# Performance work log

Measured on AMD Instinct MI355X. Metric: run time of the kernel, lower is better.

Reference implementation:

```python
import jax, jax.numpy as jnp
import numpy as np

N_ATOMS = 8192
N_EDGES = 262144
N_MOL = 128
F = 128
R = 20
CUTOFF = 5.0
L = 3
EPS = 1e-8


def setup_inputs() -> dict:
    key = jax.random.key(0)
    ks = jax.random.split(key, 20)
    sc = 0.05  # weight init scale for numerical stability
    inp = {
        "z": jax.random.randint(ks[0], (N_ATOMS,), 0, 100, dtype=jnp.int32),
        "pos": jax.random.uniform(ks[1], (N_ATOMS, 3), dtype=jnp.float32),
        "edge_src": jax.random.randint(ks[2], (N_EDGES,), 0, N_ATOMS, dtype=jnp.int32),
        "edge_dst": jax.random.randint(ks[3], (N_EDGES,), 0, N_ATOMS, dtype=jnp.int32),
        "mol_idx": jnp.sort(jax.random.randint(ks[4], (N_ATOMS,), 0, N_MOL, dtype=jnp.int32)),
        "embed": jax.random.normal(ks[5], (100, F), dtype=jnp.float32) * sc,
        "msg_w1": jax.random.normal(ks[6], (L, F, F), dtype=jnp.float32) * sc,
        "msg_b1": jnp.zeros((L, F), jnp.float32),
        "msg_w2": jax.random.normal(ks[7], (L, F, 3 * F), dtype=jnp.float32) * sc,
        "msg_b2": jnp.zeros((L, 3 * F), jnp.float32),
        "rbf_w": jax.random.normal(ks[8], (L, R, 3 * F), dtype=jnp.float32) * sc,
        "rbf_b": jnp.zeros((L, 3 * F), jnp.float32),
        "upd_u": jax.random.normal(ks[9], (L, F, F), dtype=jnp.float32) * sc,
        "upd_v": jax.random.normal(ks[10], (L, F, F), dtype=jnp.float32) * sc,
        "upd_a1": jax.random.normal(ks[11], (L, 2 * F, F), dtype=jnp.float32) * sc,
        "upd_a1b": jnp.zeros((L, F), jnp.float32),
        "upd_a2": jax.random.normal(ks[12], (L, F, 3 * F), dtype=jnp.float32) * sc,
        "upd_a2b": jnp.zeros((L, 3 * F), jnp.float32),
        "out_w1": jax.random.normal(ks[13], (F, F), dtype=jnp.float32) * sc,
        "out_b1": jnp.zeros((F,), jnp.float32),
        "out_w2": jax.random.normal(ks[14], (F, 1), dtype=jnp.float32) * sc,
        "out_b2": jnp.zeros((1,), jnp.float32),
    }
    return inp


def _painn_forward(z, pos, edge_src, edge_dst, mol_idx, embed,
                   msg_w1, msg_b1, msg_w2, msg_b2, rbf_w, rbf_b,
                   upd_u, upd_v, upd_a1, upd_a1b, upd_a2, upd_a2b,
                   out_w1, out_b1, out_w2, out_b2):
    n = z.shape[0]
    s = embed[z]                                  # [N,F]
    v = jnp.zeros((n, 3, F), s.dtype)             # [N,3,F]

    rij = pos[edge_dst] - pos[edge_src]           # [E,3]
    d = jnp.sqrt(jnp.sum(rij * rij, axis=-1) + EPS)  # [E]
    unit = rij / d[:, None]                       # [E,3]
    freq = jnp.arange(1, R + 1, dtype=s.dtype) * (jnp.pi / CUTOFF)
    rbf = jnp.sin(d[:, None] * freq[None, :]) / d[:, None]          # [E,R]
    fc = 0.5 * (jnp.cos(jnp.pi * d / CUTOFF) + 1.0) * (d < CUTOFF)  # [E]

    for l in range(L):
        # --- message block ---
        phi = jax.nn.silu(s @ msg_w1[l] + msg_b1[l]) @ msg_w2[l] + msg_b2[l]  # [N,3F]
        wfilt = (rbf @ rbf_w[l] + rbf_b[l]) * fc[:, None]                      # [E,3F]
        m = phi[edge_src] * wfilt                                              # [E,3F]
        ds_e, dvv, dvs = m[:, :F], m[:, F:2 * F], m[:, 2 * F:]
        ds = jax.ops.segment_sum(ds_e, edge_dst, num_segments=n)
        dv_e = v[edge_src] * dvv[:, None, :] + unit[:, :, None] * dvs[:, None, :]  # [E,3,F]
        dv = jax.ops.segment_sum(dv_e, edge_dst, num_segments=n)
        s = s + ds
        v = v + dv
        # --- update block ---
        uv = jnp.einsum('ncf,fg->ncg', v, upd_u[l])   # [N,3,F]
        vv = jnp.einsum('ncf,fg->ncg', v, upd_v[l])   # [N,3,F]
        vv_norm = jnp.sqrt(jnp.sum(vv * vv, axis=1) + EPS)  # [N,F]
        a = jax.nn.silu(jnp.concatenate([s, vv_norm], axis=-1) @ upd_a1[l] + upd_a1b[l])
        a = a @ upd_a2[l] + upd_a2b[l]                # [N,3F]
        a_vv, a_sv, a_ss = a[:, :F], a[:, F:2 * F], a[:, 2 * F:]
        s = s + a_ss + a_sv * jnp.sum(uv * vv, axis=1)
        v = v + a_vv[:, None, :] * uv

    atom_out = jax.nn.silu(s @ out_w1 + out_b1) @ out_w2 + out_b2  # [N,1]
    return jax.ops.segment_sum(atom_out, mol_idx, num_segments=N_MOL)  # [M,1]


def reference(z, pos, edge_src, edge_dst, mol_idx, embed,
              msg_w1, msg_b1, msg_w2, msg_b2, rbf_w, rbf_b,
              upd_u, upd_v, upd_a1, upd_a1b, upd_a2, upd_a2b,
              out_w1, out_b1, out_w2, out_b2):
    return _painn_forward(z, pos, edge_src, edge_dst, mol_idx, embed,
                          msg_w1, msg_b1, msg_w2, msg_b2, rbf_w, rbf_b,
                          upd_u, upd_v, upd_a1, upd_a1b, upd_a2, upd_a2b,
                          out_w1, out_b1, out_w2, out_b2)
```

## Files before the change

### kernel.cpp

```cpp
#include <hip/hip_runtime.h>
#include <hip/hip_bf16.h>
#include <math.h>

#define N_ATOMS 8192
#define N_EDGES 262144
#define N_MOL   128
#define FDIM    128
#define RDIM    20
#define LLAYERS 3
#define CUTOFF  5.0f
#define EPSV    1e-8f
#define PI_F    3.14159265358979323846f

typedef __attribute__((ext_vector_type(8))) short bf16x8;
typedef __attribute__((ext_vector_type(4))) float f32x4;

__device__ __forceinline__ ushort f2bf(float x) {
    uint b = __float_as_uint(x);
    return (ushort)((b + 0x7fffu + ((b >> 16) & 1u)) >> 16);
}

__global__ void k_wconv(const float* __restrict__ w1, const float* __restrict__ w2,
                        const float* __restrict__ uu, const float* __restrict__ uvw,
                        const float* __restrict__ a1, const float* __restrict__ a2,
                        const float* __restrict__ ow1, ushort* __restrict__ WT) {
    int i = blockIdx.x * 256 + threadIdx.x;
    float v;
    if (i < 49152) {
        int idx = i; int l = idx >> 14; idx &= 16383;
        int n = idx >> 7, k = idx & 127;
        v = w1[l*16384 + k*128 + n];
    } else if (i < 196608) {
        int idx = i - 49152; int l = idx / 49152; idx -= l * 49152;
        int n = idx >> 7, k = idx & 127;
        v = w2[l*49152 + k*384 + n];
    } else if (i < 294912) {
        int idx = i - 196608; int l = idx >> 15; idx &= 32767;
        int n = idx >> 7, k = idx & 127;
        v = (n < 128) ? uu[l*16384 + k*128 + n] : uvw[l*16384 + k*128 + (n-128)];
    } else if (i < 393216) {
        int idx = i - 294912; int l = idx >> 15; idx &= 32767;
        int n = idx >> 8, k = idx & 255;
        v = a1[l*32768 + k*128 + n];
    } else if (i < 540672) {
        int idx = i - 393216; int l = idx / 49152; idx -= l * 49152;
        int n = idx >> 7, k = idx & 127;
        v = a2[l*49152 + k*384 + n];
    } else {
        int idx = i - 540672;
        int n = idx >> 7, k = idx & 127;
        v = ow1[k*128 + n];
    }
    WT[i] = f2bf(v);
}

__global__ void k_embed(const int* __restrict__ z, const float* __restrict__ embed,
                        float* __restrict__ S, ushort* __restrict__ SBF) {
    int i = blockIdx.x * 256 + threadIdx.x;
    int a = i >> 7, k = i & 127;
    float v = embed[(size_t)z[a] * FDIM + k];
    S[i] = v; SBF[i] = f2bf(v);
}

__global__ void k_hist(const int* __restrict__ edst, int* __restrict__ CNT) {
    int e = blockIdx.x * 256 + threadIdx.x;
    if (e < N_EDGES) atomicAdd(&CNT[edst[e]], 1);
}

__global__ __launch_bounds__(1024) void k_scan(const int* __restrict__ CNT,
                                               int* __restrict__ OFF, int* __restrict__ CUR) {
    __shared__ int part[1024];
    int t = threadIdx.x;
    int loc[8];
    int run = 0;
    #pragma unroll
    for (int i = 0; i < 8; i++) { int c = CNT[t*8 + i]; loc[i] = run; run += c; }
    part[t] = run;
    __syncthreads();
    for (int off = 1; off < 1024; off <<= 1) {
        int v = 0;
        if (t >= off) v = part[t - off];
        __syncthreads();
        part[t] += v;
        __syncthreads();
    }
    int ebase = (t > 0) ? part[t-1] : 0;
    #pragma unroll
    for (int i = 0; i < 8; i++) { int o = ebase + loc[i]; OFF[t*8+i] = o; CUR[t*8+i] = o; }
    if (t == 1023) OFF[8192] = part[1023];
}

__global__ void k_pos(const int* __restrict__ edst, int* __restrict__ CUR,
                      int* __restrict__ POS) {
    int e = blockIdx.x * 256 + threadIdx.x;
    if (e < N_EDGES) POS[e] = atomicAdd(&CUR[edst[e]], 1);
}

__global__ void k_edges(const float* __restrict__ pos, const int* __restrict__ esrc,
                        const int* __restrict__ edst, const int* __restrict__ POS,
                        float* __restrict__ RBF, float* __restrict__ UNITFC,
                        int* __restrict__ SRCS) {
    int e = blockIdx.x * 256 + threadIdx.x;
    if (e >= N_EDGES) return;
    int s = esrc[e], d = edst[e];
    int p = POS[e];
    float rx = pos[d*3+0] - pos[s*3+0];
    float ry = pos[d*3+1] - pos[s*3+1];
    float rz = pos[d*3+2] - pos[s*3+2];
    float dd = sqrtf(rx*rx + ry*ry + rz*rz + EPSV);
    float inv = 1.0f / dd;
    float fc = (dd < CUTOFF) ? 0.5f * (cosf(dd * (PI_F / CUTOFF)) + 1.0f) : 0.0f;
    float4 u4; u4.x = rx*inv; u4.y = ry*inv; u4.z = rz*inv; u4.w = fc;
    *(float4*)&UNITFC[(size_t)p*4] = u4;
    SRCS[p] = s;
    float rb[RDIM];
    #pragma unroll
    for (int r = 0; r < RDIM; r++) {
        float freq = (float)(r + 1) * (PI_F / CUTOFF);
        rb[r] = sinf(dd * freq) * inv;
    }
    float4* out = (float4*)&RBF[(size_t)p * RDIM];
    #pragma unroll
    for (int q = 0; q < 5; q++) {
        float4 o; o.x = rb[q*4]; o.y = rb[q*4+1]; o.z = rb[q*4+2]; o.w = rb[q*4+3];
        out[q] = o;
    }
}

template<bool SILU, bool WF32, bool WB16, bool CSPLIT>
__global__ __launch_bounds__(64) void k_mgemm(
    const ushort* __restrict__ A, int lda, const ushort* __restrict__ A2, int lda2, int asplit,
    const ushort* __restrict__ BT, int ldbt, const float* __restrict__ bias,
    float* __restrict__ C, int ldc, float* __restrict__ C2, int ldc2, int csplit,
    ushort* __restrict__ CB, int ldcb, int K)
{
    int l = threadIdx.x;
    int bm = blockIdx.y * 16;
    int bn = blockIdx.x * 64;
    int lrow = l & 15, lk = (l >> 4) * 8;

    f32x4 acc[4] = {{0.f,0.f,0.f,0.f},{0.f,0.f,0.f,0.f},{0.f,0.f,0.f,0.f},{0.f,0.f,0.f,0.f}};
    for (int k0 = 0; k0 < K; k0 += 32) {
        int ka = k0 + lk;
        const ushort* Ap; int ldA;
        if (ka < asplit) { Ap = A; ldA = lda; } else { Ap = A2; ldA = lda2; ka -= asplit; }
        bf16x8 af = *(const bf16x8*)&Ap[(size_t)(bm + lrow) * ldA + ka];
        #pragma unroll
        for (int t = 0; t < 4; t++) {
            bf16x8 bfr = *(const bf16x8*)&BT[(size_t)(bn + t*16 + lrow) * ldbt + k0 + lk];
            acc[t] = __builtin_amdgcn_mfma_f32_16x16x32_bf16(af, bfr, acc[t], 0, 0, 0);
        }
    }
    #pragma unroll
    for (int t = 0; t < 4; t++) {
        int col = bn + t*16 + lrow;
        float bv = bias ? bias[col] : 0.0f;
        #pragma unroll
        for (int j = 0; j < 4; j++) {
            int row = bm + (l >> 4) * 4 + j;
            float val = acc[t][j] + bv;
            if (SILU) val = val / (1.0f + __expf(-val));
            if (WF32) {
                if (CSPLIT && col >= csplit) C2[(size_t)row * ldc2 + (col - csplit)] = val;
                else                         C [(size_t)row * ldc  + col] = val;
            }
            if (WB16) CB[(size_t)row * ldcb + col] = f2bf(val);
        }
    }
}

__global__ __launch_bounds__(192) void k_aggregate(
    const ushort* __restrict__ PHIB, const ushort* __restrict__ VBFA,
    float* __restrict__ S, ushort* __restrict__ SBF,
    float* __restrict__ V, ushort* __restrict__ VBFB,
    const float* __restrict__ RBF, const float* __restrict__ UNITFC,
    const int* __restrict__ SRCS, const int* __restrict__ OFF,
    const float* __restrict__ rbfw, const float* __restrict__ rbfb)
{
    int a = blockIdx.x;
    int tid = threadIdx.x;
    int g = tid >> 6;
    int c0 = 2 * (tid & 63);

    float2 w[RDIM];
    const float* wc = rbfw + g*128 + c0;
    #pragma unroll
    for (int r = 0; r < RDIM; r++) { w[r].x = wc[r*384]; w[r].y = wc[r*384 + 1]; }
    float2 bb; bb.x = rbfb[g*128 + c0]; bb.y = rbfb[g*128 + c0 + 1];

    __shared__ int sSrc[64];
    __shared__ float4 sRBF[320];
    __shared__ float4 sUFC[64];
    __shared__ float avs[3][128];

    int beg = OFF[a], end = OFF[a + 1];
    float2 d; d.x = 0.f; d.y = 0.f;
    float2 A0, A1, A2v;
    A0.x=A0.y=A1.x=A1.y=A2v.x=A2v.y=0.f;

    for (int p0 = beg; p0 < end; p0 += 64) {
        int n = end - p0; if (n > 64) n = 64;
        __syncthreads();
        if (tid < n) sSrc[tid] = SRCS[p0 + tid];
        for (int i = tid; i < n; i += 192)
            sUFC[i] = *(const float4*)(UNITFC + (size_t)(p0 + i) * 4);
        {
            const float4* rsrc = (const float4*)(RBF + (size_t)p0 * RDIM);
            for (int i = tid; i < n*5; i += 192) sRBF[i] = rsrc[i];
        }
        __syncthreads();

        uint phA[4], u0A[4], u1A[4], u2A[4];
        uint phB[4], u0B[4], u1B[4], u2B[4];

        auto grpLoad = [&](int base, uint* ph, uint* u0, uint* u1, uint* u2) {
            #pragma unroll
            for (int j = 0; j < 4; j++) {
                int q = base + j;
                int src = sSrc[(q < n) ? q : 0];
                size_t pb = (size_t)src * 384;
                ph[j] = *(const uint*)&PHIB[pb + g*128 + c0];
                if (g == 1) {
                    u0[j] = *(const uint*)&VBFA[pb + c0];
                    u1[j] = *(const uint*)&VBFA[pb + c0 + 128];
                    u2[j] = *(const uint*)&VBFA[pb + c0 + 256];
                }
            }
        };
        grpLoad(0, phA, u0A, u1A, u2A);
        for (int q0 = 0; q0 < n; q0 += 4) {
            if (q0 + 4 < n) grpLoad(q0 + 4, phB, u0B, u1B, u2B);
            #pragma unroll
            for (int j = 0; j < 4; j++) {
                int q = q0 + j;
                if (q >= n) break;
                float4 r0 = sRBF[q*5+0], r1 = sRBF[q*5+1], r2 = sRBF[q*5+2],
                       r3 = sRBF[q*5+3], r4 = sRBF[q*5+4];
                float4 ufc = sUFC[q];
                float2 f = bb;
                f.x += r0.x*w[0].x;   f.y += r0.x*w[0].y;
                f.x += r0.y*w[1].x;   f.y += r0.y*w[1].y;
                f.x += r0.z*w[2].x;   f.y += r0.z*w[2].y;
                f.x += r0.w*w[3].x;   f.y += r0.w*w[3].y;
                f.x += r1.x*w[4].x;   f.y += r1.x*w[4].y;
                f.x += r1.y*w[5].x;   f.y += r1.y*w[5].y;
                f.x += r1.z*w[6].x;   f.y += r1.z*w[6].y;
                f.x += r1.w*w[7].x;   f.y += r1.w*w[7].y;
                f.x += r2.x*w[8].x;   f.y += r2.x*w[8].y;
                f.x += r2.y*w[9].x;   f.y += r2.y*w[9].y;
                f.x += r2.z*w[10].x;  f.y += r2.z*w[10].y;
                f.x += r2.w*w[11].x;  f.y += r2.w*w[11].y;
                f.x += r3.x*w[12].x;  f.y += r3.x*w[12].y;
                f.x += r3.y*w[13].x;  f.y += r3.y*w[13].y;
                f.x += r3.z*w[14].x;  f.y += r3.z*w[14].y;
                f.x += r3.w*w[15].x;  f.y += r3.w*w[15].y;
                f.x += r4.x*w[16].x;  f.y += r4.x*w[16].y;
                f.x += r4.y*w[17].x;  f.y += r4.y*w[17].y;
                f.x += r4.z*w[18].x;  f.y += r4.z*w[18].y;
                f.x += r4.w*w[19].x;  f.y += r4.w*w[19].y;
                uint up = phA[j];
                float m0 = __uint_as_float(up << 16)        * (f.x * ufc.w);
                float m1 = __uint_as_float(up & 0xffff0000u) * (f.y * ufc.w);
                if (g == 0) {
                    d.x += m0; d.y += m1;
                } else if (g == 1) {
                    A0.x  += __uint_as_float(u0A[j] << 16)         * m0;
                    A0.y  += __uint_as_float(u0A[j] & 0xffff0000u) * m1;
                    A1.x  += __uint_as_float(u1A[j] << 16)         * m0;
                    A1.y  += __uint_as_float(u1A[j] & 0xffff0000u) * m1;
                    A2v.x += __uint_as_float(u2A[j] << 16)         * m0;
                    A2v.y += __uint_as_float(u2A[j] & 0xffff0000u) * m1;
                } else {
                    A0.x  += ufc.x * m0; A0.y  += ufc.x * m1;
                    A1.x  += ufc.y * m0; A1.y  += ufc.y * m1;
                    A2v.x += ufc.z * m0; A2v.y += ufc.z * m1;
                }
            }
            #pragma unroll
            for (int j = 0; j < 4; j++) {
                phA[j] = phB[j]; u0A[j] = u0B[j]; u1A[j] = u1B[j]; u2A[j] = u2B[j];
            }
        }
    }

    if (g == 1) {
        avs[0][c0] = A0.x;  avs[0][c0+1] = A0.y;
        avs[1][c0] = A1.x;  avs[1][c0+1] = A1.y;
        avs[2][c0] = A2v.x; avs[2][c0+1] = A2v.y;
    }
    __syncthreads();
    if (g == 0) {
        size_t sb = (size_t)a*128 + c0;
        float2 s2 = *(float2*)&S[sb];
        s2.x += d.x; s2.y += d.y;
        *(float2*)&S[sb] = s2;
        SBF[sb] = f2bf(s2.x); SBF[sb+1] = f2bf(s2.y);
    } else if (g == 2) {
        float own0[3] = {A0.x, A1.x, A2v.x};
        float own1[3] = {A0.y, A1.y, A2v.y};
        #pragma unroll
        for (int c = 0; c < 3; c++) {
            size_t vb = (size_t)a*384 + c*128 + c0;
            float2 vi = *(const float2*)&V[vb];
            vi.x += avs[c][c0]     + own0[c];
            vi.y += avs[c][c0 + 1] + own1[c];
            *(float2*)&V[vb] = vi;
            VBFB[vb] = f2bf(vi.x); VBFB[vb+1] = f2bf(vi.y);
        }
    }
}

__global__ void k_vvdot(const float* __restrict__ UV, const float* __restrict__ VV,
                        ushort* __restrict__ VVNB, float* __restrict__ DOT) {
    int i = blockIdx.x * 256 + threadIdx.x;
    int a = i >> 7, k = i & 127;
    size_t b = (size_t)a * 384 + k;
    float u0 = UV[b], u1 = UV[b+128], u2 = UV[b+256];
    float v0 = VV[b], v1 = VV[b+128], v2 = VV[b+256];
    VVNB[i] = f2bf(sqrtf(v0*v0 + v1*v1 + v2*v2 + EPSV));
    DOT[i] = u0*v0 + u1*v1 + u2*v2;
}

__global__ void k_update(float* __restrict__ S, ushort* __restrict__ SBF,
                         float* __restrict__ V, ushort* __restrict__ VBFA,
                         const float* __restrict__ Abuf, const float* __restrict__ UV,
                         const float* __restrict__ DOT) {
    int i = blockIdx.x * 256 + threadIdx.x;
    int a = i >> 7, k = i & 127;
    size_t b = (size_t)a * 384 + k;
    float a_vv = Abuf[b], a_sv = Abuf[b+128], a_ss = Abuf[b+256];
    float sn = S[i] + a_ss + a_sv * DOT[i];
    S[i] = sn; SBF[i] = f2bf(sn);
    float n0 = V[b]       + a_vv * UV[b];
    float n1 = V[b + 128] + a_vv * UV[b + 128];
    float n2 = V[b + 256] + a_vv * UV[b + 256];
    V[b] = n0; V[b + 128] = n1; V[b + 256] = n2;
    VBFA[b] = f2bf(n0); VBFA[b + 128] = f2bf(n1); VBFA[b + 256] = f2bf(n2);
}

__global__ __launch_bounds__(256) void k_dot(const float* __restrict__ H,
                                             const float* __restrict__ w2,
                                             const float* __restrict__ b2v,
                                             float* __restrict__ AOUT) {
    int lane = threadIdx.x & 63;
    int wv = threadIdx.x >> 6;
    int a = blockIdx.x * 4 + wv;
    const float* h = &H[(size_t)a * 128];
    float p = h[lane] * w2[lane] + h[64 + lane] * w2[64 + lane];
    #pragma unroll
    for (int off = 32; off > 0; off >>= 1) p += __shfl_down(p, off);
    if (lane == 0) AOUT[a] = p + b2v[0];
}

__global__ void k_molsum(const float* __restrict__ AOUT, const int* __restrict__ mol,
                         float* __restrict__ out) {
    __shared__ float acc[N_MOL];
    int t = threadIdx.x;
    if (t < N_MOL) acc[t] = 0.f;
    __syncthreads();
    for (int i = blockIdx.x * 256 + t; i < N_ATOMS; i += 256 * 32)
        atomicAdd(&acc[mol[i]], AOUT[i]);
    __syncthreads();
    if (t < N_MOL) atomicAdd(&out[t], acc[t]);
}

extern "C" void kernel_launch(void* const* d_in, const int* in_sizes, int n_in,
                              void* d_out, int out_size, void* d_ws, size_t ws_size,
                              hipStream_t stream) {
    const int*   z      = (const int*)d_in[0];
    const float* pos    = (const float*)d_in[1];
    const int*   esrc   = (const int*)d_in[2];
    const int*   edst   = (const int*)d_in[3];
    const int*   mol    = (const int*)d_in[4];
    const float* embed  = (const float*)d_in[5];
    const float* msg_w1 = (const float*)d_in[6];
    const float* msg_b1 = (const float*)d_in[7];
    const float* msg_w2 = (const float*)d_in[8];
    const float* msg_b2 = (const float*)d_in[9];
    const float* rbf_w  = (const float*)d_in[10];
    const float* rbf_b  = (const float*)d_in[11];
    const float* upd_u  = (const float*)d_in[12];
    const float* upd_v  = (const float*)d_in[13];
    const float* upd_a1 = (const float*)d_in[14];
    const float* upd_a1b= (const float*)d_in[15];
    const float* upd_a2 = (const float*)d_in[16];
    const float* upd_a2b= (const float*)d_in[17];
    const float* out_w1 = (const float*)d_in[18];
    const float* out_b1 = (const float*)d_in[19];
    const float* out_w2 = (const float*)d_in[20];
    const float* out_b2 = (const float*)d_in[21];

    float* ws = (float*)d_ws;
    float* S      = ws; ws += 1048576;
    float* V      = ws; ws += 3145728;
    float* ABUF   = ws; ws += 3145728;
    float* UV     = ws; ws += 3145728;
    float* DOT    = ws; ws += 1048576;
    float* RBF    = ws; ws += 5242880;
    float* UNITFC = ws; ws += 1048576;
    float* AOUT   = ws; ws += 8192;
    ushort* PHIB  = (ushort*)ws; ws += 1572864;
    ushort* VBFA  = (ushort*)ws; ws += 1572864;
    ushort* VBFB  = (ushort*)ws; ws += 1572864;
    ushort* SBF   = (ushort*)ws; ws += 524288;
    ushort* VVNB  = (ushort*)ws; ws += 524288;
    ushort* HB    = (ushort*)ws; ws += 524288;
    ushort* H2B   = (ushort*)ws; ws += 524288;
    ushort* WT    = (ushort*)ws; ws += 278528;
    int* CNT  = (int*)ws;
    int* OFF  = CNT + 8192;
    int* CUR  = OFF + 8193;
    int* POS  = CUR + 8192;
    int* SRCS = POS + N_EDGES;
    float* VV = ABUF;
    float* H  = ABUF;

    hipMemsetAsync(V, 0, 3145728 * sizeof(float), stream);
    hipMemsetAsync(VBFA, 0, 3145728 * sizeof(ushort), stream);
    hipMemsetAsync(CNT, 0, 8192 * sizeof(int), stream);

    k_wconv<<<2176, 256, 0, stream>>>(msg_w1, msg_w2, upd_u, upd_v, upd_a1, upd_a2, out_w1, WT);
    k_embed<<<4096, 256, 0, stream>>>(z, embed, S, SBF);
    k_hist<<<1024, 256, 0, stream>>>(edst, CNT);
    k_scan<<<1, 1024, 0, stream>>>(CNT, OFF, CUR);
    k_pos<<<1024, 256, 0, stream>>>(edst, CUR, POS);
    k_edges<<<1024, 256, 0, stream>>>(pos, esrc, edst, POS, RBF, UNITFC, SRCS);

    const int BIG = 1 << 30;
    for (int l = 0; l < LLAYERS; l++) {
        const ushort* W1T = WT + l*16384;
        const ushort* W2T = WT + 49152  + l*49152;
        const ushort* UVT = WT + 196608 + l*32768;
        const ushort* A1T = WT + 294912 + l*32768;
        const ushort* A2T = WT + 393216 + l*49152;

        k_mgemm<true,false,true,false><<<dim3(2,512), 64, 0, stream>>>(
            SBF, 128, nullptr, 0, BIG, W1T, 128, msg_b1 + (size_t)l*128,
            nullptr, 0, nullptr, 0, 0, HB, 128, 128);
        k_mgemm<false,false,true,false><<<dim3(6,512), 64, 0, stream>>>(
            HB, 128, nullptr, 0, BIG, W2T, 128, msg_b2 + (size_t)l*384,
            nullptr, 0, nullptr, 0, 0, PHIB, 384, 128);
        k_aggregate<<<8192, 192, 0, stream>>>(PHIB, VBFA, S, SBF, V, VBFB, RBF, UNITFC,
            SRCS, OFF, rbf_w + (size_t)l*20*384, rbf_b + (size_t)l*384);
        k_mgemm<false,true,false,true><<<dim3(4,1536), 64, 0, stream>>>(
            VBFB, 128, nullptr, 0, BIG, UVT, 128, nullptr,
            UV, 128, VV, 128, 128, nullptr, 0, 128);
        k_vvdot<<<4096, 256, 0, stream>>>(UV, VV, VVNB, DOT);
        k_mgemm<true,false,true,false><<<dim3(2,512), 64, 0, stream>>>(
            SBF, 128, VVNB, 128, 128, A1T, 256, upd_a1b + (size_t)l*128,
            nullptr, 0, nullptr, 0, 0, H2B, 128, 256);
        k_mgemm<false,true,false,false><<<dim3(6,512), 64, 0, stream>>>(
            H2B, 128, nullptr, 0, BIG, A2T, 128, upd_a2b + (size_t)l*384,
            ABUF, 384, nullptr, 0, 0, nullptr, 0, 128);
        k_update<<<4096, 256, 0, stream>>>(S, SBF, V, VBFA, ABUF, UV, DOT);
    }

    k_mgemm<true,true,false,false><<<dim3(2,512), 64, 0, stream>>>(
        SBF, 128, nullptr, 0, BIG, WT + 540672, 128, out_b1,
        H, 128, nullptr, 0, 0, nullptr, 0, 128);
    k_dot<<<2048, 256, 0, stream>>>(H, out_w2, out_b2, AOUT);
    hipMemsetAsync(d_out, 0, N_MOL * sizeof(float), stream);
    k_molsum<<<32, 256, 0, stream>>>(AOUT, mol, (float*)d_out);
}
```

Measured before the change: 720.4 us.

## Fuse per-layer GEMM chains into dedicated kernels and use planar vector layout

Replaces the generic k_mgemm launches with fused kernels. k_msg does both message MLP GEMMs with the hidden layer kept in shared memory. k_uvvv does the U/V projections together with the norm and dot epilogue. k_updmlp runs the update MLP together with the s/v update, and k_readout folds the readout dot into its GEMM. Vector features move to a plane-per-component layout, and the aggregate edge filter uses packed float2 math. The aim is to cut kernel launches and the intermediate HB/H2B/ABUF/VV round-trips through global memory, at the cost of only 512 small blocks with large accumulator arrays, which may lower occupancy.

```diff
diff --git a/kernel.cpp b/kernel.cpp
--- a/kernel.cpp
+++ b/kernel.cpp
@@ -14,6 +14,9 @@
 
 typedef __attribute__((ext_vector_type(8))) short bf16x8;
 typedef __attribute__((ext_vector_type(4))) float f32x4;
+typedef __attribute__((ext_vector_type(2))) float f32x2;
+
+#define VPLANE 1048576
 
 __device__ __forceinline__ ushort f2bf(float x) {
     uint b = __float_as_uint(x);
@@ -127,44 +130,61 @@
     }
 }
 
-template<bool SILU, bool WF32, bool WB16, bool CSPLIT>
-__global__ __launch_bounds__(64) void k_mgemm(
-    const ushort* __restrict__ A, int lda, const ushort* __restrict__ A2, int lda2, int asplit,
-    const ushort* __restrict__ BT, int ldbt, const float* __restrict__ bias,
-    float* __restrict__ C, int ldc, float* __restrict__ C2, int ldc2, int csplit,
-    ushort* __restrict__ CB, int ldcb, int K)
+__global__ __launch_bounds__(64) void k_msg(
+    const ushort* __restrict__ SBF, const ushort* __restrict__ W1T, const float* __restrict__ b1,
+    const ushort* __restrict__ W2T, const float* __restrict__ b2, ushort* __restrict__ PHIB)
 {
     int l = threadIdx.x;
-    int bm = blockIdx.y * 16;
-    int bn = blockIdx.x * 64;
+    int bm = blockIdx.x * 16;
     int lrow = l & 15, lk = (l >> 4) * 8;
-
-    f32x4 acc[4] = {{0.f,0.f,0.f,0.f},{0.f,0.f,0.f,0.f},{0.f,0.f,0.f,0.f},{0.f,0.f,0.f,0.f}};
-    for (int k0 = 0; k0 < K; k0 += 32) {
-        int ka = k0 + lk;
-        const ushort* Ap; int ldA;
-        if (ka < asplit) { Ap = A; ldA = lda; } else { Ap = A2; ldA = lda2; ka -= asplit; }
-        bf16x8 af = *(const bf16x8*)&Ap[(size_t)(bm + lrow) * ldA + ka];
-        #pragma unroll
-        for (int t = 0; t < 4; t++) {
-            bf16x8 bfr = *(const bf16x8*)&BT[(size_t)(bn + t*16 + lrow) * ldbt + k0 + lk];
-            acc[t] = __builtin_amdgcn_mfma_f32_16x16x32_bf16(af, bfr, acc[t], 0, 0, 0);
-        }
-    }
-    #pragma unroll
-    for (int t = 0; t < 4; t++) {
-        int col = bn + t*16 + lrow;
-        float bv = bias ? bias[col] : 0.0f;
+    __shared__ ushort Hs[16][136];
+
+    f32x4 acc[8];
+    #pragma unroll
+    for (int t = 0; t < 8; t++) acc[t] = (f32x4){0.f,0.f,0.f,0.f};
+    #pragma unroll
+    for (int k0 = 0; k0 < 128; k0 += 32) {
+        bf16x8 af = *(const bf16x8*)&SBF[(size_t)(bm + lrow)*128 + k0 + lk];
+        #pragma unroll
+        for (int t = 0; t < 8; t++) {
+            bf16x8 bf = *(const bf16x8*)&W1T[(size_t)(t*16 + lrow)*128 + k0 + lk];
+            acc[t] = __builtin_amdgcn_mfma_f32_16x16x32_bf16(af, bf, acc[t], 0, 0, 0);
+        }
+    }
+    #pragma unroll
+    for (int t = 0; t < 8; t++) {
+        int col = t*16 + lrow;
+        float bv = b1[col];
         #pragma unroll
         for (int j = 0; j < 4; j++) {
-            int row = bm + (l >> 4) * 4 + j;
+            int row = (l >> 4)*4 + j;
             float val = acc[t][j] + bv;
-            if (SILU) val = val / (1.0f + __expf(-val));
-            if (WF32) {
-                if (CSPLIT && col >= csplit) C2[(size_t)row * ldc2 + (col - csplit)] = val;
-                else                         C [(size_t)row * ldc  + col] = val;
-            }
-            if (WB16) CB[(size_t)row * ldcb + col] = f2bf(val);
+            val = val / (1.0f + __expf(-val));
+            Hs[row][col] = f2bf(val);
+        }
+    }
+    __syncthreads();
+
+    f32x4 acc2[24];
+    #pragma unroll
+    for (int t = 0; t < 24; t++) acc2[t] = (f32x4){0.f,0.f,0.f,0.f};
+    #pragma unroll
+    for (int k0 = 0; k0 < 128; k0 += 32) {
+        bf16x8 af = *(const bf16x8*)&Hs[lrow][k0 + lk];
+        #pragma unroll
+        for (int t = 0; t < 24; t++) {
+            bf16x8 bf = *(const bf16x8*)&W2T[(size_t)(t*16 + lrow)*128 + k0 + lk];
+            acc2[t] = __builtin_amdgcn_mfma_f32_16x16x32_bf16(af, bf, acc2[t], 0, 0, 0);
+        }
+    }
+    #pragma unroll
+    for (int t = 0; t < 24; t++) {
+        int col = t*16 + lrow;
+        float bv = b2[col];
+        #pragma unroll
+        for (int j = 0; j < 4; j++) {
+            int row = bm + (l >> 4)*4 + j;
+            PHIB[(size_t)row*384 + col] = f2bf(acc2[t][j] + bv);
         }
     }
 }
@@ -182,11 +202,11 @@
     int g = tid >> 6;
     int c0 = 2 * (tid & 63);
 
-    float2 w[RDIM];
+    f32x2 w[RDIM];
     const float* wc = rbfw + g*128 + c0;
     #pragma unroll
-    for (int r = 0; r < RDIM; r++) { w[r].x = wc[r*384]; w[r].y = wc[r*384 + 1]; }
-    float2 bb; bb.x = rbfb[g*128 + c0]; bb.y = rbfb[g*128 + c0 + 1];
+    for (int r = 0; r < RDIM; r++) { w[r] = (f32x2){wc[r*384], wc[r*384 + 1]}; }
+    f32x2 bb = (f32x2){rbfb[g*128 + c0], rbfb[g*128 + c0 + 1]};
 
     __shared__ int sSrc[64];
     __shared__ float4 sRBF[320];
@@ -194,9 +214,8 @@
     __shared__ float avs[3][128];
 
     int beg = OFF[a], end = OFF[a + 1];
-    float2 d; d.x = 0.f; d.y = 0.f;
-    float2 A0, A1, A2v;
-    A0.x=A0.y=A1.x=A1.y=A2v.x=A2v.y=0.f;
+    f32x2 d = (f32x2){0.f, 0.f};
+    f32x2 A0 = d, A1 = d, A2v = d;
 
     for (int p0 = beg; p0 < end; p0 += 64) {
         int n = end - p0; if (n > 64) n = 64;
@@ -218,12 +237,12 @@
             for (int j = 0; j < 4; j++) {
                 int q = base + j;
                 int src = sSrc[(q < n) ? q : 0];
-                size_t pb = (size_t)src * 384;
-                ph[j] = *(const uint*)&PHIB[pb + g*128 + c0];
+                size_t pb = (size_t)src * 128;
+                ph[j] = *(const uint*)&PHIB[(size_t)src*384 + g*128 + c0];
                 if (g == 1) {
                     u0[j] = *(const uint*)&VBFA[pb + c0];
-                    u1[j] = *(const uint*)&VBFA[pb + c0 + 128];
-                    u2[j] = *(const uint*)&VBFA[pb + c0 + 256];
+                    u1[j] = *(const uint*)&VBFA[pb + VPLANE + c0];
+                    u2[j] = *(const uint*)&VBFA[pb + 2*VPLANE + c0];
                 }
             }
         };
@@ -237,29 +256,29 @@
                 float4 r0 = sRBF[q*5+0], r1 = sRBF[q*5+1], r2 = sRBF[q*5+2],
                        r3 = sRBF[q*5+3], r4 = sRBF[q*5+4];
                 float4 ufc = sUFC[q];
-                float2 f = bb;
-                f.x += r0.x*w[0].x;   f.y += r0.x*w[0].y;
-                f.x += r0.y*w[1].x;   f.y += r0.y*w[1].y;
-                f.x += r0.z*w[2].x;   f.y += r0.z*w[2].y;
-                f.x += r0.w*w[3].x;   f.y += r0.w*w[3].y;
-                f.x += r1.x*w[4].x;   f.y += r1.x*w[4].y;
-                f.x += r1.y*w[5].x;   f.y += r1.y*w[5].y;
-                f.x += r1.z*w[6].x;   f.y += r1.z*w[6].y;
-                f.x += r1.w*w[7].x;   f.y += r1.w*w[7].y;
-                f.x += r2.x*w[8].x;   f.y += r2.x*w[8].y;
-                f.x += r2.y*w[9].x;   f.y += r2.y*w[9].y;
-                f.x += r2.z*w[10].x;  f.y += r2.z*w[10].y;
-                f.x += r2.w*w[11].x;  f.y += r2.w*w[11].y;
-                f.x += r3.x*w[12].x;  f.y += r3.x*w[12].y;
-                f.x += r3.y*w[13].x;  f.y += r3.y*w[13].y;
-                f.x += r3.z*w[14].x;  f.y += r3.z*w[14].y;
-                f.x += r3.w*w[15].x;  f.y += r3.w*w[15].y;
-                f.x += r4.x*w[16].x;  f.y += r4.x*w[16].y;
-                f.x += r4.y*w[17].x;  f.y += r4.y*w[17].y;
-                f.x += r4.z*w[18].x;  f.y += r4.z*w[18].y;
-                f.x += r4.w*w[19].x;  f.y += r4.w*w[19].y;
+                f32x2 f = bb;
+                f += (f32x2){r0.x, r0.x} * w[0];
+                f += (f32x2){r0.y, r0.y} * w[1];
+                f += (f32x2){r0.z, r0.z} * w[2];
+                f += (f32x2){r0.w, r0.w} * w[3];
+                f += (f32x2){r1.x, r1.x} * w[4];
+                f += (f32x2){r1.y, r1.y} * w[5];
+                f += (f32x2){r1.z, r1.z} * w[6];
+                f += (f32x2){r1.w, r1.w} * w[7];
+                f += (f32x2){r2.x, r2.x} * w[8];
+                f += (f32x2){r2.y, r2.y} * w[9];
+                f += (f32x2){r2.z, r2.z} * w[10];
+                f += (f32x2){r2.w, r2.w} * w[11];
+                f += (f32x2){r3.x, r3.x} * w[12];
+                f += (f32x2){r3.y, r3.y} * w[13];
+                f += (f32x2){r3.z, r3.z} * w[14];
+                f += (f32x2){r3.w, r3.w} * w[15];
+                f += (f32x2){r4.x, r4.x} * w[16];
+                f += (f32x2){r4.y, r4.y} * w[17];
+                f += (f32x2){r4.z, r4.z} * w[18];
+                f += (f32x2){r4.w, r4.w} * w[19];
                 uint up = phA[j];
-                float m0 = __uint_as_float(up << 16)        * (f.x * ufc.w);
+                float m0 = __uint_as_float(up << 16)         * (f.x * ufc.w);
                 float m1 = __uint_as_float(up & 0xffff0000u) * (f.y * ufc.w);
                 if (g == 0) {
                     d.x += m0; d.y += m1;
@@ -300,7 +319,7 @@
         float own1[3] = {A0.y, A1.y, A2v.y};
         #pragma unroll
         for (int c = 0; c < 3; c++) {
-            size_t vb = (size_t)a*384 + c*128 + c0;
+            size_t vb = (size_t)c*VPLANE + (size_t)a*128 + c0;
             float2 vi = *(const float2*)&V[vb];
             vi.x += avs[c][c0]     + own0[c];
             vi.y += avs[c][c0 + 1] + own1[c];
@@ -310,46 +329,178 @@
     }
 }
 
-__global__ void k_vvdot(const float* __restrict__ UV, const float* __restrict__ VV,
-                        ushort* __restrict__ VVNB, float* __restrict__ DOT) {
-    int i = blockIdx.x * 256 + threadIdx.x;
-    int a = i >> 7, k = i & 127;
-    size_t b = (size_t)a * 384 + k;
-    float u0 = UV[b], u1 = UV[b+128], u2 = UV[b+256];
-    float v0 = VV[b], v1 = VV[b+128], v2 = VV[b+256];
-    VVNB[i] = f2bf(sqrtf(v0*v0 + v1*v1 + v2*v2 + EPSV));
-    DOT[i] = u0*v0 + u1*v1 + u2*v2;
-}
-
-__global__ void k_update(float* __restrict__ S, ushort* __restrict__ SBF,
-                         float* __restrict__ V, ushort* __restrict__ VBFA,
-                         const float* __restrict__ Abuf, const float* __restrict__ UV,
-                         const float* __restrict__ DOT) {
-    int i = blockIdx.x * 256 + threadIdx.x;
-    int a = i >> 7, k = i & 127;
-    size_t b = (size_t)a * 384 + k;
-    float a_vv = Abuf[b], a_sv = Abuf[b+128], a_ss = Abuf[b+256];
-    float sn = S[i] + a_ss + a_sv * DOT[i];
-    S[i] = sn; SBF[i] = f2bf(sn);
-    float n0 = V[b]       + a_vv * UV[b];
-    float n1 = V[b + 128] + a_vv * UV[b + 128];
-    float n2 = V[b + 256] + a_vv * UV[b + 256];
-    V[b] = n0; V[b + 128] = n1; V[b + 256] = n2;
-    VBFA[b] = f2bf(n0); VBFA[b + 128] = f2bf(n1); VBFA[b + 256] = f2bf(n2);
-}
-
-__global__ __launch_bounds__(256) void k_dot(const float* __restrict__ H,
-                                             const float* __restrict__ w2,
-                                             const float* __restrict__ b2v,
-                                             float* __restrict__ AOUT) {
-    int lane = threadIdx.x & 63;
-    int wv = threadIdx.x >> 6;
-    int a = blockIdx.x * 4 + wv;
-    const float* h = &H[(size_t)a * 128];
-    float p = h[lane] * w2[lane] + h[64 + lane] * w2[64 + lane];
-    #pragma unroll
-    for (int off = 32; off > 0; off >>= 1) p += __shfl_down(p, off);
-    if (lane == 0) AOUT[a] = p + b2v[0];
+__global__ __launch_bounds__(128) void k_uvvv(
+    const ushort* __restrict__ VBFB, const ushort* __restrict__ UVT,
+    float* __restrict__ UV, ushort* __restrict__ VVNB, float* __restrict__ DOT)
+{
+    int l = threadIdx.x & 63, w = threadIdx.x >> 6;
+    int bm = blockIdx.x * 16;
+    int lrow = l & 15, lk = (l >> 4) * 8;
+
+    f32x4 au[3][4], av[3][4];
+    #pragma unroll
+    for (int c = 0; c < 3; c++)
+        #pragma unroll
+        for (int t = 0; t < 4; t++) {
+            au[c][t] = (f32x4){0.f,0.f,0.f,0.f};
+            av[c][t] = (f32x4){0.f,0.f,0.f,0.f};
+        }
+
+    #pragma unroll
+    for (int k0 = 0; k0 < 128; k0 += 32) {
+        bf16x8 af[3];
+        #pragma unroll
+        for (int c = 0; c < 3; c++)
+            af[c] = *(const bf16x8*)&VBFB[(size_t)c*VPLANE + (size_t)(bm + lrow)*128 + k0 + lk];
+        #pragma unroll
+        for (int t = 0; t < 4; t++) {
+            int nu = (4*w + t)*16 + lrow;
+            bf16x8 bu = *(const bf16x8*)&UVT[(size_t)nu*128 + k0 + lk];
+            bf16x8 bv = *(const bf16x8*)&UVT[(size_t)(nu + 128)*128 + k0 + lk];
+            #pragma unroll
+            for (int c = 0; c < 3; c++) {
+                au[c][t] = __builtin_amdgcn_mfma_f32_16x16x32_bf16(af[c], bu, au[c][t], 0, 0, 0);
+                av[c][t] = __builtin_amdgcn_mfma_f32_16x16x32_bf16(af[c], bv, av[c][t], 0, 0, 0);
+            }
+        }
+    }
+
+    #pragma unroll
+    for (int t = 0; t < 4; t++) {
+        int k = (4*w + t)*16 + lrow;
+        #pragma unroll
+        for (int j = 0; j < 4; j++) {
+            int a = bm + (l >> 4)*4 + j;
+            float u0 = au[0][t][j], u1 = au[1][t][j], u2 = au[2][t][j];
+            float v0 = av[0][t][j], v1 = av[1][t][j], v2 = av[2][t][j];
+            size_t base = (size_t)a*128 + k;
+            UV[base]            = u0;
+            UV[VPLANE + base]   = u1;
+            UV[2*VPLANE + base] = u2;
+            VVNB[base] = f2bf(sqrtf(v0*v0 + v1*v1 + v2*v2 + EPSV));
+            DOT[base]  = u0*v0 + u1*v1 + u2*v2;
+        }
+    }
+}
+
+__global__ __launch_bounds__(64) void k_updmlp(
+    const ushort* __restrict__ SBF_in, const ushort* __restrict__ VVNB,
+    const ushort* __restrict__ A1T, const float* __restrict__ a1b,
+    const ushort* __restrict__ A2T, const float* __restrict__ a2b,
+    const float* __restrict__ DOT, const float* __restrict__ UV,
+    float* __restrict__ S, ushort* __restrict__ SBF,
+    float* __restrict__ V, ushort* __restrict__ VBFA)
+{
+    int l = threadIdx.x;
+    int bm = blockIdx.x * 16;
+    int lrow = l & 15, lk = (l >> 4) * 8;
+    __shared__ ushort Hs[16][136];
+
+    f32x4 acc[8];
+    #pragma unroll
+    for (int t = 0; t < 8; t++) acc[t] = (f32x4){0.f,0.f,0.f,0.f};
+    #pragma unroll
+    for (int k0 = 0; k0 < 256; k0 += 32) {
+        int ka = k0 + lk;
+        bf16x8 af = (ka < 128)
+            ? *(const bf16x8*)&SBF_in[(size_t)(bm + lrow)*128 + ka]
+            : *(const bf16x8*)&VVNB[(size_t)(bm + lrow)*128 + ka - 128];
+        #pragma unroll
+        for (int t = 0; t < 8; t++) {
+            bf16x8 bf = *(const bf16x8*)&A1T[(size_t)(t*16 + lrow)*256 + k0 + lk];
+            acc[t] = __builtin_amdgcn_mfma_f32_16x16x32_bf16(af, bf, acc[t], 0, 0, 0);
+        }
+    }
+    #pragma unroll
+    for (int t = 0; t < 8; t++) {
+        int col = t*16 + lrow;
+        float bv = a1b[col];
+        #pragma unroll
+        for (int j = 0; j < 4; j++) {
+            int row = (l >> 4)*4 + j;
+            float val = acc[t][j] + bv;
+            val = val / (1.0f + __expf(-val));
+            Hs[row][col] = f2bf(val);
+        }
+    }
+    __syncthreads();
+
+    f32x4 acc2[24];
+    #pragma unroll
+    for (int t = 0; t < 24; t++) acc2[t] = (f32x4){0.f,0.f,0.f,0.f};
+    #pragma unroll
+    for (int k0 = 0; k0 < 128; k0 += 32) {
+        bf16x8 af = *(const bf16x8*)&Hs[lrow][k0 + lk];
+        #pragma unroll
+        for (int t = 0; t < 24; t++) {
+            bf16x8 bf = *(const bf16x8*)&A2T[(size_t)(t*16 + lrow)*128 + k0 + lk];
+            acc2[t] = __builtin_amdgcn_mfma_f32_16x16x32_bf16(af, bf, acc2[t], 0, 0, 0);
+        }
+    }
+
+    #pragma unroll
+    for (int t = 0; t < 8; t++) {
+        int k = t*16 + lrow;
+        float b_vv = a2b[k], b_sv = a2b[128 + k], b_ss = a2b[256 + k];
+        #pragma unroll
+        for (int j = 0; j < 4; j++) {
+            int a = bm + (l >> 4)*4 + j;
+            size_t base = (size_t)a*128 + k;
+            float vv = acc2[t][j]      + b_vv;
+            float sv = acc2[t + 8][j]  + b_sv;
+            float ss = acc2[t + 16][j] + b_ss;
+            float sn = S[base] + ss + sv * DOT[base];
+            S[base] = sn; SBF[base] = f2bf(sn);
+            #pragma unroll
+            for (int c = 0; c < 3; c++) {
+                size_t vb = (size_t)c*VPLANE + base;
+                float nv = V[vb] + vv * UV[vb];
+                V[vb] = nv; VBFA[vb] = f2bf(nv);
+            }
+        }
+    }
+}
+
+__global__ __launch_bounds__(64) void k_readout(
+    const ushort* __restrict__ SBF, const ushort* __restrict__ OW1T,
+    const float* __restrict__ b1, const float* __restrict__ w2,
+    const float* __restrict__ b2v, float* __restrict__ AOUT)
+{
+    int l = threadIdx.x;
+    int bm = blockIdx.x * 16;
+    int lrow = l & 15, lk = (l >> 4) * 8;
+    __shared__ float Hs[16][132];
+
+    f32x4 acc[8];
+    #pragma unroll
+    for (int t = 0; t < 8; t++) acc[t] = (f32x4){0.f,0.f,0.f,0.f};
+    #pragma unroll
+    for (int k0 = 0; k0 < 128; k0 += 32) {
+        bf16x8 af = *(const bf16x8*)&SBF[(size_t)(bm + lrow)*128 + k0 + lk];
+        #pragma unroll
+        for (int t = 0; t < 8; t++) {
+            bf16x8 bf = *(const bf16x8*)&OW1T[(size_t)(t*16 + lrow)*128 + k0 + lk];
+            acc[t] = __builtin_amdgcn_mfma_f32_16x16x32_bf16(af, bf, acc[t], 0, 0, 0);
+        }
+    }
+    #pragma unroll
+    for (int t = 0; t < 8; t++) {
+        int col = t*16 + lrow;
+        float bv = b1[col];
+        #pragma unroll
+        for (int j = 0; j < 4; j++) {
+            int row = (l >> 4)*4 + j;
+            float val = acc[t][j] + bv;
+            Hs[row][col] = val / (1.0f + __expf(-val));
+        }
+    }
+    __syncthreads();
+    if (l < 16) {
+        float s = b2v[0];
+        #pragma unroll 8
+        for (int k = 0; k < 128; k++) s += Hs[l][k] * w2[k];
+        AOUT[bm + l] = s;
+    }
 }
 
 __global__ void k_molsum(const float* __restrict__ AOUT, const int* __restrict__ mol,
@@ -393,7 +544,6 @@
     float* ws = (float*)d_ws;
     float* S      = ws; ws += 1048576;
     float* V      = ws; ws += 3145728;
-    float* ABUF   = ws; ws += 3145728;
     float* UV     = ws; ws += 3145728;
     float* DOT    = ws; ws += 1048576;
     float* RBF    = ws; ws += 5242880;
@@ -404,16 +554,12 @@
     ushort* VBFB  = (ushort*)ws; ws += 1572864;
     ushort* SBF   = (ushort*)ws; ws += 524288;
     ushort* VVNB  = (ushort*)ws; ws += 524288;
-    ushort* HB    = (ushort*)ws; ws += 524288;
-    ushort* H2B   = (ushort*)ws; ws += 524288;
     ushort* WT    = (ushort*)ws; ws += 278528;
     int* CNT  = (int*)ws;
     int* OFF  = CNT + 8192;
     int* CUR  = OFF + 8193;
     int* POS  = CUR + 8192;
     int* SRCS = POS + N_EDGES;
-    float* VV = ABUF;
-    float* H  = ABUF;
 
     hipMemsetAsync(V, 0, 3145728 * sizeof(float), stream);
     hipMemsetAsync(VBFA, 0, 3145728 * sizeof(ushort), stream);
@@ -426,7 +572,6 @@
     k_pos<<<1024, 256, 0, stream>>>(edst, CUR, POS);
     k_edges<<<1024, 256, 0, stream>>>(pos, esrc, edst, POS, RBF, UNITFC, SRCS);
 
-    const int BIG = 1 << 30;
     for (int l = 0; l < LLAYERS; l++) {
         const ushort* W1T = WT + l*16384;
         const ushort* W2T = WT + 49152  + l*49152;
@@ -434,31 +579,16 @@
         const ushort* A1T = WT + 294912 + l*32768;
         const ushort* A2T = WT + 393216 + l*49152;
 
-        k_mgemm<true,false,true,false><<<dim3(2,512), 64, 0, stream>>>(
-            SBF, 128, nullptr, 0, BIG, W1T, 128, msg_b1 + (size_t)l*128,
-            nullptr, 0, nullptr, 0, 0, HB, 128, 128);
-        k_mgemm<false,false,true,false><<<dim3(6,512), 64, 0, stream>>>(
-            HB, 128, nullptr, 0, BIG, W2T, 128, msg_b2 + (size_t)l*384,
-            nullptr, 0, nullptr, 0, 0, PHIB, 384, 128);
+        k_msg<<<512, 64, 0, stream>>>(SBF, W1T, msg_b1 + (size_t)l*128,
+                                      W2T, msg_b2 + (size_t)l*384, PHIB);
         k_aggregate<<<8192, 192, 0, stream>>>(PHIB, VBFA, S, SBF, V, VBFB, RBF, UNITFC,
             SRCS, OFF, rbf_w + (size_t)l*20*384, rbf_b + (size_t)l*384);
-        k_mgemm<false,true,false,true><<<dim3(4,1536), 64, 0, stream>>>(
-            VBFB, 128, nullptr, 0, BIG, UVT, 128, nullptr,
-            UV, 128, VV, 128, 128, nullptr, 0, 128);
-        k_vvdot<<<4096, 256, 0, stream>>>(UV, VV, VVNB, DOT);
-        k_mgemm<true,false,true,false><<<dim3(2,512), 64, 0, stream>>>(
-            SBF, 128, VVNB, 128, 128, A1T, 256, upd_a1b + (size_t)l*128,
-            nullptr, 0, nullptr, 0, 0, H2B, 128, 256);
-        k_mgemm<false,true,false,false><<<dim3(6,512), 64, 0, stream>>>(
-            H2B, 128, nullptr, 0, BIG, A2T, 128, upd_a2b + (size_t)l*384,
-            ABUF, 384, nullptr, 0, 0, nullptr, 0, 128);
-        k_update<<<4096, 256, 0, stream>>>(S, SBF, V, VBFA, ABUF, UV, DOT);
-    }
-
-    k_mgemm<true,true,false,false><<<dim3(2,512), 64, 0, stream>>>(
-        SBF, 128, nullptr, 0, BIG, WT + 540672, 128, out_b1,
-        H, 128, nullptr, 0, 0, nullptr, 0, 128);
-    k_dot<<<2048, 256, 0, stream>>>(H, out_w2, out_b2, AOUT);
+        k_uvvv<<<512, 128, 0, stream>>>(VBFB, UVT, UV, VVNB, DOT);
+        k_updmlp<<<512, 64, 0, stream>>>(SBF, VVNB, A1T, upd_a1b + (size_t)l*128,
+            A2T, upd_a2b + (size_t)l*384, DOT, UV, S, SBF, V, VBFA);
+    }
+
+    k_readout<<<512, 64, 0, stream>>>(SBF, WT + 540672, out_b1, out_w2, out_b2, AOUT);
     hipMemsetAsync(d_out, 0, N_MOL * sizeof(float), stream);
     k_molsum<<<32, 256, 0, stream>>>(AOUT, mol, (float*)d_out);
 }
```

Measured after the change: 764.3 us. 1.06x slower.
